# Kernel tuning notes

Hardware: AMD Instinct MI355X
Metric: run time of the kernel (lower is better)

The kernel has to match this reference:

```python
import jax, jax.numpy as jnp
import numpy as np

N = 50000   # nodes
E = 800000  # edges (avg degree 16)
G = 64      # graphs in batch
H = 4       # attention heads
D = 128     # hidden dim per head (= hidden_dim)
V = 128     # embedding vocab (input_dim)
NEG_SLOPE = 0.2

def setup_inputs() -> dict:
    key = jax.random.key(0)
    ks = jax.random.split(key, 12)
    s = 0.05
    return {
        "feats": jax.random.randint(ks[0], (N,), 0, V),
        "src": jax.random.randint(ks[1], (E,), 0, N),
        "dst": jax.random.randint(ks[2], (E,), 0, N),
        "graph_ids": jnp.sort(jax.random.randint(ks[3], (N,), 0, G)),
        "emb": jax.random.normal(ks[4], (V, D)) * s,
        "W1": jax.random.normal(ks[5], (D, H * D)) * s,
        "b1": jax.random.normal(ks[6], (H * D,)) * s,
        "a1": jax.random.normal(ks[7], (H, D)) * s,
        "W2": jax.random.normal(ks[8], (D, H * D)) * s,
        "b2": jax.random.normal(ks[9], (H * D,)) * s,
        "a2": jax.random.normal(ks[10], (H, D)) * s,
        "Wreg": jax.random.normal(ks[11], (1, D)) * s,
    }

def gatv2_layer(x, W, b, a, src, dst):
    # shared-weight GATv2: h = Wx + b, split into heads -> [N,H,D]
    h = (x @ W + b).reshape(-1, H, D)
    hs = h[src]                      # [E,H,D] source feats per edge
    hd = h[dst]                      # [E,H,D] dest feats per edge
    e = jax.nn.leaky_relu(hs + hd, NEG_SLOPE)
    logits = jnp.einsum('ehd,hd->eh', e, a)          # [E,H]
    # edge softmax over incoming edges of each dst node
    m = jax.ops.segment_max(logits, dst, num_segments=N)
    m = jnp.where(jnp.isfinite(m), m, 0.0)           # empty segments -> 0 (unused)
    ex = jnp.exp(logits - m[dst])
    denom = jax.ops.segment_sum(ex, dst, num_segments=N)
    alpha = ex / denom[dst]                          # [E,H]
    rst = jax.ops.segment_sum(alpha[:, :, None] * hs, dst, num_segments=N)  # [N,H,D]
    return rst.mean(axis=1)          # .mean(dim=1) over heads -> [N,D]

def reference(feats, src, dst, graph_ids, emb, W1, b1, a1, W2, b2, a2, Wreg):
    x = emb[feats]                                   # embedding lookup [N,D]
    x = gatv2_layer(x, W1, b1, a1, src, dst)         # layer 1 (dropout=0)
    x = gatv2_layer(x, W2, b2, a2, src, dst)         # layer 2
    pooled = jax.ops.segment_sum(x, graph_ids, num_segments=G)  # SumPooling [G,D]
    return pooled @ Wreg.T                           # Linear bias=False -> [G,1]
```

## Files before the change

### kernel.cpp

```cpp
#include <hip/hip_runtime.h>
#include <hip/hip_bf16.h>

#define N_NODES 50000
#define N_EDGES 800000
#define G_GRAPHS 64
#define H_HEADS 4
#define D_DIM 128
#define HD 512
#define V_VOCAB 128
#define NEG_SLOPE 0.2f

typedef float f32x2v __attribute__((ext_vector_type(2)));
typedef float f32x4 __attribute__((ext_vector_type(4)));
typedef short s16x8 __attribute__((ext_vector_type(8)));
typedef _Float16 h16x2 __attribute__((ext_vector_type(2)));

static __device__ __forceinline__ unsigned short f2b(float f) {
    union { float f; unsigned int i; } x; x.f = f;
    unsigned int r = x.i + 0x7fffu + ((x.i >> 16) & 1u);
    return (unsigned short)(r >> 16);
}
static __device__ __forceinline__ h16x2 u2h2(unsigned int u) {
    union { unsigned int u; h16x2 h; } c; c.u = u; return c.h;
}
static __device__ __forceinline__ unsigned int h22u(h16x2 h) {
    union { unsigned int u; h16x2 h; } c; c.h = h; return c.u;
}
static __device__ __forceinline__ h16x2 packf2(float lo, float hi) {
    union { __fp16 __attribute__((ext_vector_type(2))) p; h16x2 h; } c;
    c.p = __builtin_amdgcn_cvt_pkrtz(lo, hi);
    return c.h;
}

#if __has_builtin(__builtin_amdgcn_cvt_scalef32_pk_f16_fp8)
static __device__ __forceinline__ void fp8x4_to_h16(unsigned int u, h16x2& h0, h16x2& h1) {
    auto r0 = __builtin_amdgcn_cvt_scalef32_pk_f16_fp8((int)u, 1.0f, false);
    auto r1 = __builtin_amdgcn_cvt_scalef32_pk_f16_fp8((int)u, 1.0f, true);
    union { decltype(r0) p; h16x2 h; } c0, c1;
    c0.p = r0; c1.p = r1;
    h0 = c0.h; h1 = c1.h;
}
#else
static __device__ __forceinline__ void fp8x4_to_h16(unsigned int u, h16x2& h0, h16x2& h1) {
    f32x2v lo = __builtin_amdgcn_cvt_pk_f32_fp8(u, false);
    f32x2v hi = __builtin_amdgcn_cvt_pk_f32_fp8(u, true);
    h0 = packf2(lo.x, lo.y);
    h1 = packf2(hi.x, hi.y);
}
#endif

template<int CTRL>
static __device__ __forceinline__ float dpp_add(float v) {
    union { float f; int i; } a, b;
    a.f = v;
    b.i = __builtin_amdgcn_mov_dpp(a.i, CTRL, 0xF, 0xF, true);
    return v + b.f;
}
static __device__ __forceinline__ float row16_sum(float p) {
    p = dpp_add<0xB1>(p);
    p = dpp_add<0x4E>(p);
    p = dpp_add<0x141>(p);
    p = dpp_add<0x140>(p);
    return p;
}

__global__ void hist_kernel(const int* __restrict__ dst, int* __restrict__ counts,
                            float* __restrict__ pool) {
    if (blockIdx.x == 0 && threadIdx.x < G_GRAPHS) pool[threadIdx.x] = 0.f;
    int i = blockIdx.x * blockDim.x + threadIdx.x;
    if (i < N_EDGES) atomicAdd(&counts[dst[i]], 1);
}

__global__ void __launch_bounds__(256) scan1_kernel(const int* __restrict__ counts,
                                                    int* __restrict__ offsets,
                                                    int* __restrict__ bsum) {
    __shared__ int buf[256];
    int t = threadIdx.x, b = blockIdx.x;
    int i0 = (b * 256 + t) * 4;
    int v[4], c[4], s = 0;
    #pragma unroll
    for (int j = 0; j < 4; j++) {
        int idx = i0 + j;
        v[j] = (idx < N_NODES) ? counts[idx] : 0;
        s += v[j];
        c[j] = s;
    }
    buf[t] = s;
    __syncthreads();
    for (int off = 1; off < 256; off <<= 1) {
        int add = (t >= off) ? buf[t - off] : 0;
        __syncthreads();
        buf[t] += add;
        __syncthreads();
    }
    int ebase = (t > 0) ? buf[t - 1] : 0;
    #pragma unroll
    for (int j = 0; j < 4; j++) {
        int idx = i0 + j;
        if (idx < N_NODES) offsets[idx + 1] = ebase + c[j];
    }
    if (t == 0) bsum[b] = buf[255];
}

__global__ void __launch_bounds__(256) scan23_kernel(const int* __restrict__ counts,
                                                     int* __restrict__ offsets,
                                                     const int* __restrict__ bsum,
                                                     int* __restrict__ cursor) {
    __shared__ int sbase;
    int t = threadIdx.x, b = blockIdx.x;
    if (t < 64) {
        int v = (t < b) ? bsum[t] : 0;
        #pragma unroll
        for (int off = 1; off < 64; off <<= 1) v += __shfl_xor(v, off);
        if (t == 0) sbase = v;
    }
    __syncthreads();
    int base = sbase;
    int i0 = (b * 256 + t) * 4;
    #pragma unroll
    for (int j = 0; j < 4; j++) {
        int idx = i0 + j;
        if (idx < N_NODES) {
            int e = offsets[idx + 1] + base;
            offsets[idx + 1] = e;
            cursor[idx] = e - counts[idx];
        }
    }
    if (b == 0 && t == 0) offsets[0] = 0;
}

__global__ void scatter_kernel(const int* __restrict__ src, const int* __restrict__ dst,
                               int* __restrict__ cursor, int* __restrict__ csr_src) {
    int i = blockIdx.x * blockDim.x + threadIdx.x;
    if (i < N_EDGES) {
        int d = dst[i];
        int pos = atomicAdd(&cursor[d], 1);
        csr_src[pos] = src[i];
    }
}

#define PREP_M1_BLOCKS   256
#define PREP_WSZ_BLOCKS  256
#define PREP_CNT_BLOCKS  196
__global__ void __launch_bounds__(256) prep_kernel(const float* __restrict__ emb,
                                                   const float* __restrict__ W1,
                                                   float* __restrict__ M1,
                                                   const float* __restrict__ W2,
                                                   unsigned short* __restrict__ Wb,
                                                   int* __restrict__ counts,
                                                   int* __restrict__ done) {
    int b = blockIdx.x;
    if (b < PREP_M1_BLOCKS) {
        int idx = b * 256 + threadIdx.x;
        int v = idx >> 9, c = idx & 511;
        float acc = 0.f;
        for (int k = 0; k < 128; k++)
            acc += emb[v * 128 + k] * W1[k * 512 + c];
        M1[idx] = acc;
    } else if (b < PREP_M1_BLOCKS + PREP_WSZ_BLOCKS) {
        int idx = (b - PREP_M1_BLOCKS) * 256 + threadIdx.x;
        int j = idx & 7, c = (idx >> 3) & 511, qq = idx >> 12;
        Wb[idx] = f2b(W2[(qq * 8 + j) * 512 + c]);
    } else {
        int idx = (b - PREP_M1_BLOCKS - PREP_WSZ_BLOCKS) * 256 + threadIdx.x;
        if (idx < N_NODES) counts[idx] = 0;
        if (idx == 0) *done = 0;
    }
}

__global__ void gather_kernel(const int* __restrict__ feats, const float* __restrict__ M1,
                              const float* __restrict__ b1,
                              unsigned int* __restrict__ h) {
    int tid = blockIdx.x * blockDim.x + threadIdx.x;
    int i0 = tid * 8;
    int n = i0 >> 9, c = i0 & 511;
    if (n >= N_NODES) return;
    int f = feats[n];
    const float* mrow = &M1[f * 512 + c];
    float v[8];
    #pragma unroll
    for (int j = 0; j < 8; j++) v[j] = mrow[j] + b1[c + j];
    uint2 o;
    o.x = __builtin_amdgcn_cvt_pk_fp8_f32(v[0], v[1], 0, false);
    o.x = __builtin_amdgcn_cvt_pk_fp8_f32(v[2], v[3], o.x, true);
    o.y = __builtin_amdgcn_cvt_pk_fp8_f32(v[4], v[5], 0, false);
    o.y = __builtin_amdgcn_cvt_pk_fp8_f32(v[6], v[7], o.y, true);
    *reinterpret_cast<uint2*>(&h[i0 >> 2]) = o;
}

template<bool WRITE_DOTS>
__global__ void __launch_bounds__(256) gat_kernel(const unsigned int* __restrict__ h,
                                                  const int* __restrict__ offsets,
                                                  const int* __restrict__ csr_src,
                                                  const float* __restrict__ a,
                                                  const float* __restrict__ wreg,
                                                  unsigned short* __restrict__ x,
                                                  float* __restrict__ dots) {
    int wid = threadIdx.x >> 6;
    int lane = threadIdx.x & 63;
    int n = blockIdx.x * 4 + wid;
    if (n >= N_NODES) return;
    n = __builtin_amdgcn_readfirstlane(n);
    int row_s = __builtin_amdgcn_readfirstlane(offsets[n]);
    int row_e = __builtin_amdgcn_readfirstlane(offsets[n + 1]);
    int cnt = row_e - row_s;
    int voff = lane * 2;

    h16x2 hd2[4], a06[4], a04[4], acc2[4];
    float pd;
    {
        uint2 hv = *reinterpret_cast<const uint2*>(&h[(unsigned)n * 128u + voff]);
        fp8x4_to_h16(hv.x, hd2[0], hd2[1]);
        fp8x4_to_h16(hv.y, hd2[2], hd2[3]);
        float4 av0 = *reinterpret_cast<const float4*>(&a[lane * 8]);
        float4 av1 = *reinterpret_cast<const float4*>(&a[lane * 8 + 4]);
        float aa[8] = {av0.x, av0.y, av0.z, av0.w, av1.x, av1.y, av1.z, av1.w};
        const float L2E = 1.4426950408889634f;
        #pragma unroll
        for (int k = 0; k < 4; k++) {
            a06[k][0] = (_Float16)(aa[2*k]   * (0.6f * L2E));
            a06[k][1] = (_Float16)(aa[2*k+1] * (0.6f * L2E));
            a04[k][0] = (_Float16)(aa[2*k]   * (0.4f * L2E));
            a04[k][1] = (_Float16)(aa[2*k+1] * (0.4f * L2E));
            acc2[k][0] = (_Float16)0.f; acc2[k][1] = (_Float16)0.f;
        }
        float s = 0.f;
        #pragma unroll
        for (int k = 0; k < 4; k++) s = __builtin_amdgcn_fdot2(hd2[k], a06[k], s, false);
        pd = row16_sum(s);
    }

    auto ld = [&](int ii) {
        int s = __builtin_amdgcn_readfirstlane(csr_src[row_s + ii]);
        return *reinterpret_cast<const uint2*>(&h[(unsigned)s * 128u + voff]);
    };

    float den = 0.f;
    uint2 rA = make_uint2(0, 0), rB = make_uint2(0, 0);
    if (cnt > 0) rA = ld(0);
    if (cnt > 1) rB = ld(1);

    const float C1 = 0.69314718f, C2 = 0.24022651f, C3 = 0.05550411f;

    auto process = [&](uint2 sv) {
        h16x2 hs[4];
        fp8x4_to_h16(sv.x, hs[0], hs[1]);
        fp8x4_to_h16(sv.y, hs[2], hs[3]);
        float p0 = 0.f, p1 = 0.f;
        #pragma unroll
        for (int k = 0; k < 2; k++) {
            h16x2 t2 = hs[k] + hd2[k];
            h16x2 at2 = u2h2(h22u(t2) & 0x7FFF7FFFu);
            p0 = __builtin_amdgcn_fdot2(hs[k], a06[k], p0, false);
            p0 = __builtin_amdgcn_fdot2(at2, a04[k], p0, false);
        }
        #pragma unroll
        for (int k = 2; k < 4; k++) {
            h16x2 t2 = hs[k] + hd2[k];
            h16x2 at2 = u2h2(h22u(t2) & 0x7FFF7FFFu);
            p1 = __builtin_amdgcn_fdot2(hs[k], a06[k], p1, false);
            p1 = __builtin_amdgcn_fdot2(at2, a04[k], p1, false);
        }
        float p = row16_sum(p0 + p1) + pd;
        float w = fmaf(p, fmaf(p, fmaf(p, C3, C2), C1), 1.f);
        den += w;
        h16x2 w2 = packf2(w, w);
        #pragma unroll
        for (int k = 0; k < 4; k++) acc2[k] = w2 * hs[k] + acc2[k];
    };

    for (int i = 0; i < cnt; i += 2) {
        {
            uint2 cur = rA;
            rA = ld(min(i + 2, cnt - 1));
            process(cur);
        }
        if (i + 1 < cnt) {
            uint2 cur = rB;
            rB = ld(min(i + 3, cnt - 1));
            process(cur);
        }
    }

    float inv = (den > 0.f) ? 0.25f / den : 0.f;
    float out8[8];
    #pragma unroll
    for (int j = 0; j < 8; j++) {
        float r = (float)acc2[j >> 1][j & 1] * inv;
        r += __shfl_xor(r, 16);
        r += __shfl_xor(r, 32);
        out8[j] = r;
    }
    if constexpr (WRITE_DOTS) {
        int d0 = (lane & 15) * 8;
        float4 wv0 = *reinterpret_cast<const float4*>(&wreg[d0]);
        float4 wv1 = *reinterpret_cast<const float4*>(&wreg[d0 + 4]);
        float pdot = out8[0] * wv0.x + out8[1] * wv0.y + out8[2] * wv0.z + out8[3] * wv0.w
                   + out8[4] * wv1.x + out8[5] * wv1.y + out8[6] * wv1.z + out8[7] * wv1.w;
        pdot = row16_sum(pdot);
        if (lane == 0) dots[n] = pdot;
    } else {
        if (lane < 16) {
            union { unsigned short u[8]; uint4 v; } o;
            #pragma unroll
            for (int j = 0; j < 8; j++) o.u[j] = f2b(out8[j]);
            *reinterpret_cast<uint4*>(&x[(unsigned)n * 128u + lane * 8]) = o.v;
        }
    }
}

__global__ void __launch_bounds__(256) gemm_kernel(const unsigned short* __restrict__ x,
                                                   const unsigned short* __restrict__ Wb,
                                                   const float* __restrict__ bias,
                                                   unsigned char* __restrict__ hout) {
    int w = threadIdx.x >> 6, l = threadIdx.x & 63;
    int rb = blockIdx.x * 64 + w * 16;
    int cb = blockIdx.y * 64;
    int lr = l & 15, lq = l >> 4;
    f32x4 acc[4] = {};
    int arow = rb + lr;
    bool rok = arow < N_NODES;
    #pragma unroll
    for (int s = 0; s < 4; s++) {
        s16x8 afr = {};
        if (rok) afr = *reinterpret_cast<const s16x8*>(&x[(size_t)arow * 128 + s * 32 + lq * 8]);
        #pragma unroll
        for (int sub = 0; sub < 4; sub++) {
            s16x8 bfr = *reinterpret_cast<const s16x8*>(
                &Wb[(((size_t)(s * 4 + lq) * 512) + cb + sub * 16 + lr) << 3]);
            acc[sub] = __builtin_amdgcn_mfma_f32_16x16x32_bf16(bfr, afr, acc[sub], 0, 0, 0);
        }
    }
    if (!rok) return;
    #pragma unroll
    for (int sub = 0; sub < 4; sub++) {
        int col0 = cb + sub * 16 + lq * 4;
        float4 bb = *reinterpret_cast<const float4*>(&bias[col0]);
        unsigned int pk = __builtin_amdgcn_cvt_pk_fp8_f32(acc[sub][0] + bb.x,
                                                          acc[sub][1] + bb.y, 0, false);
        pk = __builtin_amdgcn_cvt_pk_fp8_f32(acc[sub][2] + bb.z,
                                             acc[sub][3] + bb.w, pk, true);
        *reinterpret_cast<unsigned int*>(&hout[(size_t)arow * 512 + col0]) = pk;
    }
}

__global__ void __launch_bounds__(256) pool64_kernel(const float* __restrict__ dots,
                                                     const int* __restrict__ gid,
                                                     float* __restrict__ pool,
                                                     int* __restrict__ done,
                                                     float* __restrict__ out) {
    int wave = (blockIdx.x * blockDim.x + threadIdx.x) >> 6;
    int lane = threadIdx.x & 63;
    int n0 = wave * 64;
    if (n0 < N_NODES) {
        int n = n0 + lane;
        int nc = min(n, N_NODES - 1);
        int g = gid[nc];
        float v = (n < N_NODES) ? dots[n] : 0.f;
        int g0 = __shfl(g, 0);
        bool uni = __all(g == g0);
        if (uni) {
            v += __shfl_xor(v, 1);
            v += __shfl_xor(v, 2);
            v += __shfl_xor(v, 4);
            v += __shfl_xor(v, 8);
            v += __shfl_xor(v, 16);
            v += __shfl_xor(v, 32);
            if (lane == 0) atomicAdd(&pool[g0], v);
        } else {
            if (n < N_NODES) atomicAdd(&pool[g], v);
        }
    }
    __threadfence();
    __syncthreads();
    __shared__ int amlast;
    if (threadIdx.x == 0)
        amlast = (atomicAdd(done, 1) == (int)gridDim.x - 1) ? 1 : 0;
    __syncthreads();
    if (amlast && threadIdx.x < G_GRAPHS) {
        out[threadIdx.x] = atomicAdd(&pool[threadIdx.x], 0.f);
    }
}

extern "C" void kernel_launch(void* const* d_in, const int* in_sizes, int n_in,
                              void* d_out, int out_size, void* d_ws, size_t ws_size,
                              hipStream_t stream) {
    const int* feats = (const int*)d_in[0];
    const int* src   = (const int*)d_in[1];
    const int* dst   = (const int*)d_in[2];
    const int* gids  = (const int*)d_in[3];
    const float* emb  = (const float*)d_in[4];
    const float* W1   = (const float*)d_in[5];
    const float* b1   = (const float*)d_in[6];
    const float* a1   = (const float*)d_in[7];
    const float* W2   = (const float*)d_in[8];
    const float* b2   = (const float*)d_in[9];
    const float* a2   = (const float*)d_in[10];
    const float* wreg = (const float*)d_in[11];
    float* out = (float*)d_out;

    char* ws = (char*)d_ws;
    size_t off = 0;
    auto alloc = [&](size_t bytes) -> void* {
        void* p = ws + off;
        off = (off + bytes + 255) & ~(size_t)255;
        return p;
    };
    int*   counts  = (int*)alloc((size_t)N_NODES * 4);
    int*   offsets = (int*)alloc((size_t)(N_NODES + 1) * 4);
    int*   cursor  = (int*)alloc((size_t)N_NODES * 4);
    int*   csr_src = (int*)alloc((size_t)N_EDGES * 4);
    int*   bsum    = (int*)alloc(64 * 4);
    int*   done    = (int*)alloc(4);
    float* M1      = (float*)alloc((size_t)V_VOCAB * HD * 4);
    unsigned int*   h  = (unsigned int*)alloc((size_t)N_NODES * HD);
    unsigned short* x  = (unsigned short*)alloc((size_t)N_NODES * D_DIM * 2);
    unsigned short* Wb = (unsigned short*)alloc((size_t)D_DIM * HD * 2);
    float* dots    = (float*)alloc((size_t)N_NODES * 4);
    float* pool    = (float*)alloc((size_t)G_GRAPHS * 4);

    prep_kernel<<<PREP_M1_BLOCKS + PREP_WSZ_BLOCKS + PREP_CNT_BLOCKS, 256, 0, stream>>>(
        emb, W1, M1, W2, Wb, counts, done);
    hist_kernel<<<(N_EDGES + 255) / 256, 256, 0, stream>>>(dst, counts, pool);
    scan1_kernel<<<64, 256, 0, stream>>>(counts, offsets, bsum);
    scan23_kernel<<<64, 256, 0, stream>>>(counts, offsets, bsum, cursor);
    scatter_kernel<<<(N_EDGES + 255) / 256, 256, 0, stream>>>(src, dst, cursor, csr_src);

    gather_kernel<<<(N_NODES * HD / 8) / 256, 256, 0, stream>>>(feats, M1, b1, h);

    gat_kernel<false><<<(N_NODES + 3) / 4, 256, 0, stream>>>(h, offsets, csr_src, a1,
                                                             wreg, x, dots);
    gemm_kernel<<<dim3((N_NODES + 63) / 64, 8), 256, 0, stream>>>(x, Wb, b2, (unsigned char*)h);
    gat_kernel<true><<<(N_NODES + 3) / 4, 256, 0, stream>>>(h, offsets, csr_src, a2,
                                                            wreg, x, dots);

    pool64_kernel<<<(N_NODES / 64 + 4) / 4, 256, 0, stream>>>(dots, gids, pool, done, out);
}
```

Before: 335.2 us.

## Fuse preprocessing launches and merge the two scan passes with a grid barrier

Collapses six preprocessing launches into a memset plus three kernels. The weight prep and the degree histogram now run in one kernel, and the CSR scatter and embedding gather share another. The two-pass scan becomes a single kernel that uses an atomic-flag grid barrier across its 64 blocks, and counts are zeroed with hipMemsetAsync. This cuts launch overhead and inter-kernel gaps, but the spin barrier assumes all 64 blocks are co-resident.

Result: no change. 332.4 us (-0.8%).

```diff
diff --git a/kernel.cpp b/kernel.cpp
--- a/kernel.cpp
+++ b/kernel.cpp
@@ -64,17 +64,44 @@
     return p;
 }
 
-__global__ void hist_kernel(const int* __restrict__ dst, int* __restrict__ counts,
-                            float* __restrict__ pool) {
-    if (blockIdx.x == 0 && threadIdx.x < G_GRAPHS) pool[threadIdx.x] = 0.f;
-    int i = blockIdx.x * blockDim.x + threadIdx.x;
-    if (i < N_EDGES) atomicAdd(&counts[dst[i]], 1);
-}
-
-__global__ void __launch_bounds__(256) scan1_kernel(const int* __restrict__ counts,
+#define MEGA_M1_BLOCKS   256
+#define MEGA_WSZ_BLOCKS  256
+#define MEGA_HIST_BLOCKS ((N_EDGES + 255) / 256)
+__global__ void __launch_bounds__(256) mega_kernel(const float* __restrict__ emb,
+                                                   const float* __restrict__ W1,
+                                                   float* __restrict__ M1,
+                                                   const float* __restrict__ W2,
+                                                   unsigned short* __restrict__ Wb,
+                                                   const int* __restrict__ dst,
+                                                   int* __restrict__ counts,
+                                                   float* __restrict__ pool) {
+    int b = blockIdx.x;
+    if (b < MEGA_M1_BLOCKS) {
+        int idx = b * 256 + threadIdx.x;
+        int v = idx >> 9, c = idx & 511;
+        float acc = 0.f;
+        for (int k = 0; k < 128; k++)
+            acc += emb[v * 128 + k] * W1[k * 512 + c];
+        M1[idx] = acc;
+    } else if (b < MEGA_M1_BLOCKS + MEGA_WSZ_BLOCKS) {
+        int idx = (b - MEGA_M1_BLOCKS) * 256 + threadIdx.x;
+        int j = idx & 7, c = (idx >> 3) & 511, qq = idx >> 12;
+        Wb[idx] = f2b(W2[(qq * 8 + j) * 512 + c]);
+    } else {
+        int hb = b - MEGA_M1_BLOCKS - MEGA_WSZ_BLOCKS;
+        if (hb == 0 && threadIdx.x < G_GRAPHS) pool[threadIdx.x] = 0.f;
+        int i = hb * 256 + threadIdx.x;
+        if (i < N_EDGES) atomicAdd(&counts[dst[i]], 1);
+    }
+}
+
+__global__ void __launch_bounds__(256) scanf_kernel(const int* __restrict__ counts,
                                                     int* __restrict__ offsets,
-                                                    int* __restrict__ bsum) {
+                                                    int* __restrict__ cursor,
+                                                    int* __restrict__ bsum,
+                                                    int* __restrict__ flag) {
     __shared__ int buf[256];
+    __shared__ int sbase;
     int t = threadIdx.x, b = blockIdx.x;
     int i0 = (b * 256 + t) * 4;
     int v[4], c[4], s = 0;
@@ -94,98 +121,68 @@
         __syncthreads();
     }
     int ebase = (t > 0) ? buf[t - 1] : 0;
-    #pragma unroll
-    for (int j = 0; j < 4; j++) {
-        int idx = i0 + j;
-        if (idx < N_NODES) offsets[idx + 1] = ebase + c[j];
-    }
-    if (t == 0) bsum[b] = buf[255];
-}
-
-__global__ void __launch_bounds__(256) scan23_kernel(const int* __restrict__ counts,
-                                                     int* __restrict__ offsets,
-                                                     const int* __restrict__ bsum,
-                                                     int* __restrict__ cursor) {
-    __shared__ int sbase;
-    int t = threadIdx.x, b = blockIdx.x;
+    if (t == 0) {
+        bsum[b] = buf[255];
+        __threadfence();
+        atomicAdd(flag, 1);
+        while (atomicAdd(flag, 0) < 64) __builtin_amdgcn_s_sleep(8);
+    }
+    __syncthreads();
     if (t < 64) {
-        int v = (t < b) ? bsum[t] : 0;
-        #pragma unroll
-        for (int off = 1; off < 64; off <<= 1) v += __shfl_xor(v, off);
-        if (t == 0) sbase = v;
+        int vv = (t < b) ? atomicAdd(&bsum[t], 0) : 0;
+        #pragma unroll
+        for (int off = 1; off < 64; off <<= 1) vv += __shfl_xor(vv, off);
+        if (t == 0) sbase = vv;
     }
     __syncthreads();
     int base = sbase;
-    int i0 = (b * 256 + t) * 4;
     #pragma unroll
     for (int j = 0; j < 4; j++) {
         int idx = i0 + j;
         if (idx < N_NODES) {
-            int e = offsets[idx + 1] + base;
+            int e = base + ebase + c[j];
             offsets[idx + 1] = e;
-            cursor[idx] = e - counts[idx];
+            cursor[idx] = e - v[j];
         }
     }
     if (b == 0 && t == 0) offsets[0] = 0;
 }
 
-__global__ void scatter_kernel(const int* __restrict__ src, const int* __restrict__ dst,
-                               int* __restrict__ cursor, int* __restrict__ csr_src) {
-    int i = blockIdx.x * blockDim.x + threadIdx.x;
-    if (i < N_EDGES) {
-        int d = dst[i];
-        int pos = atomicAdd(&cursor[d], 1);
-        csr_src[pos] = src[i];
-    }
-}
-
-#define PREP_M1_BLOCKS   256
-#define PREP_WSZ_BLOCKS  256
-#define PREP_CNT_BLOCKS  196
-__global__ void __launch_bounds__(256) prep_kernel(const float* __restrict__ emb,
-                                                   const float* __restrict__ W1,
-                                                   float* __restrict__ M1,
-                                                   const float* __restrict__ W2,
-                                                   unsigned short* __restrict__ Wb,
-                                                   int* __restrict__ counts,
-                                                   int* __restrict__ done) {
+#define SG_SCAT_BLOCKS ((N_EDGES + 255) / 256)
+#define SG_GATH_BLOCKS (N_NODES * HD / 8 / 256)
+__global__ void __launch_bounds__(256) scatgath_kernel(const int* __restrict__ src,
+                                                       const int* __restrict__ dst,
+                                                       int* __restrict__ cursor,
+                                                       int* __restrict__ csr_src,
+                                                       const int* __restrict__ feats,
+                                                       const float* __restrict__ M1,
+                                                       const float* __restrict__ b1,
+                                                       unsigned int* __restrict__ h) {
     int b = blockIdx.x;
-    if (b < PREP_M1_BLOCKS) {
-        int idx = b * 256 + threadIdx.x;
-        int v = idx >> 9, c = idx & 511;
-        float acc = 0.f;
-        for (int k = 0; k < 128; k++)
-            acc += emb[v * 128 + k] * W1[k * 512 + c];
-        M1[idx] = acc;
-    } else if (b < PREP_M1_BLOCKS + PREP_WSZ_BLOCKS) {
-        int idx = (b - PREP_M1_BLOCKS) * 256 + threadIdx.x;
-        int j = idx & 7, c = (idx >> 3) & 511, qq = idx >> 12;
-        Wb[idx] = f2b(W2[(qq * 8 + j) * 512 + c]);
+    if (b < SG_SCAT_BLOCKS) {
+        int i = b * 256 + threadIdx.x;
+        if (i < N_EDGES) {
+            int d = dst[i];
+            int pos = atomicAdd(&cursor[d], 1);
+            csr_src[pos] = src[i];
+        }
     } else {
-        int idx = (b - PREP_M1_BLOCKS - PREP_WSZ_BLOCKS) * 256 + threadIdx.x;
-        if (idx < N_NODES) counts[idx] = 0;
-        if (idx == 0) *done = 0;
-    }
-}
-
-__global__ void gather_kernel(const int* __restrict__ feats, const float* __restrict__ M1,
-                              const float* __restrict__ b1,
-                              unsigned int* __restrict__ h) {
-    int tid = blockIdx.x * blockDim.x + threadIdx.x;
-    int i0 = tid * 8;
-    int n = i0 >> 9, c = i0 & 511;
-    if (n >= N_NODES) return;
-    int f = feats[n];
-    const float* mrow = &M1[f * 512 + c];
-    float v[8];
-    #pragma unroll
-    for (int j = 0; j < 8; j++) v[j] = mrow[j] + b1[c + j];
-    uint2 o;
-    o.x = __builtin_amdgcn_cvt_pk_fp8_f32(v[0], v[1], 0, false);
-    o.x = __builtin_amdgcn_cvt_pk_fp8_f32(v[2], v[3], o.x, true);
-    o.y = __builtin_amdgcn_cvt_pk_fp8_f32(v[4], v[5], 0, false);
-    o.y = __builtin_amdgcn_cvt_pk_fp8_f32(v[6], v[7], o.y, true);
-    *reinterpret_cast<uint2*>(&h[i0 >> 2]) = o;
+        int tid = (b - SG_SCAT_BLOCKS) * 256 + threadIdx.x;
+        int i0 = tid * 8;
+        int n = i0 >> 9, c = i0 & 511;
+        if (n >= N_NODES) return;
+        int f = feats[n];
+        const float* mrow = &M1[f * 512 + c];
+        float v[8];
+        #pragma unroll
+        for (int j = 0; j < 8; j++) v[j] = mrow[j] + b1[c + j];
+        uint2 o;
+        o.x = __builtin_amdgcn_cvt_pk_fp8_f32(v[0], v[1], 0, false);
+        o.x = __builtin_amdgcn_cvt_pk_fp8_f32(v[2], v[3], o.x, true);
+        o.y = __builtin_amdgcn_cvt_pk_fp8_f32(v[4], v[5], 0, false);
+        o.y = __builtin_amdgcn_cvt_pk_fp8_f32(v[6], v[7], o.y, true);
+        *reinterpret_cast<uint2*>(&h[i0 >> 2]) = o;
+    }
 }
 
 template<bool WRITE_DOTS>
@@ -406,12 +403,13 @@
         off = (off + bytes + 255) & ~(size_t)255;
         return p;
     };
-    int*   counts  = (int*)alloc((size_t)N_NODES * 4);
+    int*   counts  = (int*)alloc((size_t)N_NODES * 4 + 8);
+    int*   flag    = counts + N_NODES;
+    int*   done    = counts + N_NODES + 1;
     int*   offsets = (int*)alloc((size_t)(N_NODES + 1) * 4);
     int*   cursor  = (int*)alloc((size_t)N_NODES * 4);
     int*   csr_src = (int*)alloc((size_t)N_EDGES * 4);
     int*   bsum    = (int*)alloc(64 * 4);
-    int*   done    = (int*)alloc(4);
     float* M1      = (float*)alloc((size_t)V_VOCAB * HD * 4);
     unsigned int*   h  = (unsigned int*)alloc((size_t)N_NODES * HD);
     unsigned short* x  = (unsigned short*)alloc((size_t)N_NODES * D_DIM * 2);
@@ -419,14 +417,13 @@
     float* dots    = (float*)alloc((size_t)N_NODES * 4);
     float* pool    = (float*)alloc((size_t)G_GRAPHS * 4);
 
-    prep_kernel<<<PREP_M1_BLOCKS + PREP_WSZ_BLOCKS + PREP_CNT_BLOCKS, 256, 0, stream>>>(
-        emb, W1, M1, W2, Wb, counts, done);
-    hist_kernel<<<(N_EDGES + 255) / 256, 256, 0, stream>>>(dst, counts, pool);
-    scan1_kernel<<<64, 256, 0, stream>>>(counts, offsets, bsum);
-    scan23_kernel<<<64, 256, 0, stream>>>(counts, offsets, bsum, cursor);
-    scatter_kernel<<<(N_EDGES + 255) / 256, 256, 0, stream>>>(src, dst, cursor, csr_src);
-
-    gather_kernel<<<(N_NODES * HD / 8) / 256, 256, 0, stream>>>(feats, M1, b1, h);
+    hipMemsetAsync(counts, 0, (size_t)N_NODES * 4 + 8, stream);
+
+    mega_kernel<<<MEGA_M1_BLOCKS + MEGA_WSZ_BLOCKS + MEGA_HIST_BLOCKS, 256, 0, stream>>>(
+        emb, W1, M1, W2, Wb, dst, counts, pool);
+    scanf_kernel<<<64, 256, 0, stream>>>(counts, offsets, cursor, bsum, flag);
+    scatgath_kernel<<<SG_SCAT_BLOCKS + SG_GATH_BLOCKS, 256, 0, stream>>>(
+        src, dst, cursor, csr_src, feats, M1, b1, h);
 
     gat_kernel<false><<<(N_NODES + 3) / 4, 256, 0, stream>>>(h, offsets, csr_src, a1,
                                                              wreg, x, dots);
```
